# Kernel tuning notes

Measured on AMD Instinct MI355X. Metric: run time of the kernel, lower is better.

Reference implementation:

```python
import jax, jax.numpy as jnp
import numpy as np

N_NODES = 50000
N_EDGES = 800000
D_IN = 128
HID = 128
N_CLS = 5
BN_EPS = 1e-5


def setup_inputs() -> dict:
    key = jax.random.key(0)
    ks = jax.random.split(key, 8)

    def lin(k, fan_in, shape):
        return (jax.random.normal(k, shape, jnp.float32) / np.sqrt(fan_in)).astype(jnp.float32)

    inp = {
        'x': jax.random.normal(ks[0], (N_NODES, D_IN), jnp.float32),
        'edge_index': jax.random.randint(ks[1], (2, N_EDGES), 0, N_NODES, dtype=jnp.int64),
        'W0': lin(ks[2], D_IN, (D_IN, HID)), 'b0': jnp.zeros((HID,), jnp.float32),
        'g0': jnp.ones((HID,), jnp.float32), 'be0': jnp.zeros((HID,), jnp.float32),
        'W1': lin(ks[3], HID, (HID, HID)), 'b1': jnp.zeros((HID,), jnp.float32),
        'g1': jnp.ones((HID,), jnp.float32), 'be1': jnp.zeros((HID,), jnp.float32),
        'W2': lin(ks[4], HID, (HID, HID)), 'b2': jnp.zeros((HID,), jnp.float32),
        'g2': jnp.ones((HID,), jnp.float32), 'be2': jnp.zeros((HID,), jnp.float32),
        'cW1': lin(ks[5], HID, (HID, HID // 2)), 'cb1': jnp.zeros((HID // 2,), jnp.float32),
        'cW2': lin(ks[6], HID // 2, (HID // 2, N_CLS)), 'cb2': jnp.zeros((N_CLS,), jnp.float32),
    }
    return inp


def _gcn_conv(x, src, dst, W, b):
    # H = D~^{-1/2} (A+I) D~^{-1/2} X W + b  (Kipf & Welling / PyG GCNConv)
    h = x @ W                                           # [N, out]
    deg = jnp.zeros((N_NODES,), h.dtype).at[dst].add(1.0) + 1.0  # degree incl. self-loop
    dinv = jax.lax.rsqrt(deg)                           # D~^{-1/2}
    norm = dinv[src] * dinv[dst]                        # [E]
    agg = jnp.zeros_like(h).at[dst].add(h[src] * norm[:, None])
    agg = agg + h * (dinv * dinv)[:, None]              # self-loop term
    return agg + b


def _batchnorm(x, gamma, beta):
    # training-mode BatchNorm1d over the node dimension
    mean = x.mean(axis=0)
    var = x.var(axis=0)
    return gamma * (x - mean) * jax.lax.rsqrt(var + BN_EPS) + beta


def reference(x, edge_index, W0, b0, g0, be0, W1, b1, g1, be1, W2, b2, g2, be2,
              cW1, cb1, cW2, cb2):
    src, dst = edge_index[0], edge_index[1]
    for W, b, g, be in ((W0, b0, g0, be0), (W1, b1, g1, be1), (W2, b2, g2, be2)):
        x = _gcn_conv(x, src, dst, W, b)
        x = _batchnorm(x, g, be)
        x = jax.nn.relu(x)
        # dropout: identity (eval / deterministic reference)
    pooled = x.mean(axis=0, keepdims=True)              # [1, HID]
    h = jax.nn.relu(pooled @ cW1 + cb1)
    return h @ cW2 + cb2                                # [1, N_CLS]
```

## Files before the change

### kernel.cpp

```cpp
#include <hip/hip_runtime.h>
#include <hip/hip_fp16.h>
#include <cstdint>
#include <cstddef>

#define D 128
#define NAGG 2048
#define SCAN_BLOCKS 256


__global__ void count_kernel(const int* __restrict__ ei, int* __restrict__ counts, int E) {
  for (int e = blockIdx.x * blockDim.x + threadIdx.x; e < E; e += gridDim.x * blockDim.x) {
    int d = ei[(size_t)E + e];
    atomicAdd(&counts[d], 1);
  }
}


__global__ __launch_bounds__(256) void scan1_kernel(const int* __restrict__ counts,
                                                    int* __restrict__ blocksums, int N) {
  __shared__ int red[256];
  const int b = blockIdx.x, t = threadIdx.x;
  const int chunk = (N + SCAN_BLOCKS - 1) / SCAN_BLOCKS;
  const int lo = b * chunk, hi = min(lo + chunk, N);
  int s = 0;
  for (int i = lo + t; i < hi; i += 256) s += counts[i];
  red[t] = s;
  __syncthreads();
  for (int off = 128; off > 0; off >>= 1) {
    if (t < off) red[t] += red[t + off];
    __syncthreads();
  }
  if (t == 0) blocksums[b] = red[0];
}

__global__ __launch_bounds__(256) void scan2_kernel(int* __restrict__ blocksums) {
  __shared__ int part[256];
  const int t = threadIdx.x;
  part[t] = blocksums[t];
  __syncthreads();
  for (int off = 1; off < 256; off <<= 1) {
    int v = part[t];
    int u = (t >= off) ? part[t - off] : 0;
    __syncthreads();
    part[t] = v + u;
    __syncthreads();
  }
  blocksums[t] = (t == 0) ? 0 : part[t - 1];
}

__global__ __launch_bounds__(256) void scan3_kernel(const int* __restrict__ counts,
                                                    const int* __restrict__ blocksums,
                                                    int* __restrict__ row_ptr,
                                                    int* __restrict__ cursor,
                                                    float* __restrict__ dinv, int N) {
  __shared__ int tsum[256];
  const int b = blockIdx.x, t = threadIdx.x;
  const int chunk = (N + SCAN_BLOCKS - 1) / SCAN_BLOCKS;
  const int lo = b * chunk, hi = min(lo + chunk, N);
  const int tchunk = (chunk + 255) >> 8;
  const int tlo = lo + t * tchunk, thi = min(tlo + tchunk, hi);
  int s = 0;
  for (int i = tlo; i < thi; i++) s += counts[i];
  tsum[t] = s;
  __syncthreads();
  for (int off = 1; off < 256; off <<= 1) {
    int v = tsum[t];
    int u = (t >= off) ? tsum[t - off] : 0;
    __syncthreads();
    tsum[t] = v + u;
    __syncthreads();
  }
  int run = blocksums[b] + ((t == 0) ? 0 : tsum[t - 1]);
  for (int i = tlo; i < thi; i++) {
    int c = counts[i];
    row_ptr[i] = run; cursor[i] = run; run += c;
    dinv[i] = rsqrtf((float)c + 1.0f);
  }
  if (b == SCAN_BLOCKS - 1 && t == 255) row_ptr[N] = blocksums[b] + tsum[255];
}


__global__ void fill_kernel(const int* __restrict__ ei, int* __restrict__ cursor,
                            int* __restrict__ col, int E) {
  for (int e = blockIdx.x * blockDim.x + threadIdx.x; e < E; e += gridDim.x * blockDim.x) {
    int s = ei[e];
    int d = ei[(size_t)E + e];
    int pos = atomicAdd(&cursor[d], 1);
    atomicExch(&col[pos], s);
  }
}


template <typename T>
__device__ inline float4 load4f(const T* p);
template <>
__device__ inline float4 load4f<float>(const float* p) { return *(const float4*)p; }
template <>
__device__ inline float4 load4f<__half>(const __half* p) {
  float2 a = __half22float2(*(const __half2*)p);
  float2 b = __half22float2(*(const __half2*)(p + 2));
  return make_float4(a.x, a.y, b.x, b.y);
}

template <typename T>
__global__ __launch_bounds__(256) void gemm_kernel(
    const T* __restrict__ A, const float* __restrict__ Wm,
    const float* __restrict__ scale, const float* __restrict__ shift,
    const float* __restrict__ rowscale, __half* __restrict__ out, int M) {
  __shared__ float At[32][132];
  __shared__ float Wl[32][128];
  const int tid = threadIdx.x;
  const int tr = tid >> 4;
  const int tc = tid & 15;
  const int bm = blockIdx.x * 128;

  float acc[8][8];
#pragma unroll
  for (int r = 0; r < 8; r++)
#pragma unroll
    for (int c = 0; c < 8; c++) acc[r][c] = 0.f;

  for (int k0 = 0; k0 < 128; k0 += 32) {
    __syncthreads();
#pragma unroll
    for (int i = 0; i < 4; i++) {
      int idx = tid + i * 256;
      int row = idx >> 3;
      int kk = (idx & 7) << 2;
      int gr = bm + row;
      float4 v = make_float4(0.f, 0.f, 0.f, 0.f);
      if (gr < M) {
        v = load4f(A + (size_t)gr * D + k0 + kk);
        if (scale) {
          int c = k0 + kk;
          v.x = fmaxf(fmaf(v.x, scale[c + 0], shift[c + 0]), 0.f);
          v.y = fmaxf(fmaf(v.y, scale[c + 1], shift[c + 1]), 0.f);
          v.z = fmaxf(fmaf(v.z, scale[c + 2], shift[c + 2]), 0.f);
          v.w = fmaxf(fmaf(v.w, scale[c + 3], shift[c + 3]), 0.f);
        }
      }
      At[kk + 0][row] = v.x; At[kk + 1][row] = v.y;
      At[kk + 2][row] = v.z; At[kk + 3][row] = v.w;
    }
#pragma unroll
    for (int i = 0; i < 4; i++) {
      int idx = tid + i * 256;
      int kk = idx >> 5;
      int c4 = (idx & 31) << 2;
      *(float4*)&Wl[kk][c4] = *(const float4*)(Wm + (size_t)(k0 + kk) * D + c4);
    }
    __syncthreads();

#pragma unroll 4
    for (int kk = 0; kk < 32; kk++) {
      float4 alo = *(const float4*)&At[kk][tr * 8];
      float4 ahi = *(const float4*)&At[kk][tr * 8 + 4];
      float4 blo = *(const float4*)&Wl[kk][tc * 4];
      float4 bhi = *(const float4*)&Wl[kk][tc * 4 + 64];
      float a[8] = {alo.x, alo.y, alo.z, alo.w, ahi.x, ahi.y, ahi.z, ahi.w};
      float b[8] = {blo.x, blo.y, blo.z, blo.w, bhi.x, bhi.y, bhi.z, bhi.w};
#pragma unroll
      for (int r = 0; r < 8; r++)
#pragma unroll
        for (int c = 0; c < 8; c++) acc[r][c] = fmaf(a[r], b[c], acc[r][c]);
    }
  }

#pragma unroll
  for (int r = 0; r < 8; r++) {
    int gr = bm + tr * 8 + r;
    if (gr < M) {
      float dv = rowscale[gr];
      __half2 h0 = __floats2half2_rn(acc[r][0] * dv, acc[r][1] * dv);
      __half2 h1 = __floats2half2_rn(acc[r][2] * dv, acc[r][3] * dv);
      __half2 h2 = __floats2half2_rn(acc[r][4] * dv, acc[r][5] * dv);
      __half2 h3 = __floats2half2_rn(acc[r][6] * dv, acc[r][7] * dv);
      __half2* p0 = (__half2*)(out + (size_t)gr * D + tc * 4);
      __half2* p1 = (__half2*)(out + (size_t)gr * D + tc * 4 + 64);
      p0[0] = h0; p0[1] = h1;
      p1[0] = h2; p1[1] = h3;
    }
  }
}


__global__ __launch_bounds__(256) void agg_kernel(
    const __half* __restrict__ hp, const int* __restrict__ row_ptr, const int* __restrict__ col,
    const float* __restrict__ dinv, const float* __restrict__ bias,
    __half* __restrict__ y, float* __restrict__ pstats, int M) {
  const int tid = threadIdx.x;
  const int wave = tid >> 6;
  const int lane = tid & 63;
  const float bx = bias[lane * 2];
  const float by = bias[lane * 2 + 1];
  float sx = 0.f, sy = 0.f, qx = 0.f, qy = 0.f;

  for (int n = blockIdx.x * 4 + wave; n < M; n += gridDim.x * 4) {
    const int beg = row_ptr[n];
    const int end = row_ptr[n + 1];
    const float dn = dinv[n];
    float2 self = __half22float2(*(const __half2*)(hp + (size_t)n * D + lane * 2));
    float ax = self.x, ay = self.y;
#pragma unroll 4
    for (int e = beg; e < end; e++) {
      int s = col[e];
      float2 hv = __half22float2(*(const __half2*)(hp + (size_t)s * D + lane * 2));
      ax += hv.x; ay += hv.y;
    }
    ax = fmaf(ax, dn, bx);
    ay = fmaf(ay, dn, by);
    *(__half2*)(y + (size_t)n * D + lane * 2) = __floats2half2_rn(ax, ay);
    sx += ax; sy += ay;
    qx = fmaf(ax, ax, qx); qy = fmaf(ay, ay, qy);
  }

  __shared__ float ps[4][128];
  ps[wave][lane * 2] = sx; ps[wave][lane * 2 + 1] = sy;
  __syncthreads();
  if (tid < 128) {
    float s = ps[0][tid] + ps[1][tid] + ps[2][tid] + ps[3][tid];
    pstats[(size_t)blockIdx.x * 256 + tid] = s;
  }
  __syncthreads();
  ps[wave][lane * 2] = qx; ps[wave][lane * 2 + 1] = qy;
  __syncthreads();
  if (tid < 128) {
    float s = ps[0][tid] + ps[1][tid] + ps[2][tid] + ps[3][tid];
    pstats[(size_t)blockIdx.x * 256 + 128 + tid] = s;
  }
}


__global__ void bnred_kernel(const float* __restrict__ pstats, const float* __restrict__ g,
                             const float* __restrict__ be, float* __restrict__ scale,
                             float* __restrict__ shift, float invN) {
  const int c = blockIdx.x;
  const int tid = threadIdx.x;
  float s = 0.f, q = 0.f;
  for (int b = tid; b < NAGG; b += 256) {
    s += pstats[(size_t)b * 256 + c];
    q += pstats[(size_t)b * 256 + 128 + c];
  }
  __shared__ float rs[256], rq[256];
  rs[tid] = s; rq[tid] = q;
  __syncthreads();
  for (int off = 128; off > 0; off >>= 1) {
    if (tid < off) { rs[tid] += rs[tid + off]; rq[tid] += rq[tid + off]; }
    __syncthreads();
  }
  if (tid == 0) {
    float mean = rs[0] * invN;
    float var = rq[0] * invN - mean * mean;
    float sc = g[c] * rsqrtf(var + 1e-5f);
    scale[c] = sc;
    shift[c] = be[c] - mean * sc;
  }
}


__global__ __launch_bounds__(256) void pool_kernel(
    const __half* __restrict__ y, const float* __restrict__ scale, const float* __restrict__ shift,
    float* __restrict__ ppool, int M) {
  const int tid = threadIdx.x;
  const int wave = tid >> 6;
  const int lane = tid & 63;
  const float scx = scale[lane * 2], scy = scale[lane * 2 + 1];
  const float shx = shift[lane * 2], shy = shift[lane * 2 + 1];
  float sx = 0.f, sy = 0.f;
  for (int n = blockIdx.x * 4 + wave; n < M; n += gridDim.x * 4) {
    float2 v = __half22float2(*(const __half2*)(y + (size_t)n * D + lane * 2));
    sx += fmaxf(fmaf(v.x, scx, shx), 0.f);
    sy += fmaxf(fmaf(v.y, scy, shy), 0.f);
  }
  __shared__ float ps[4][128];
  ps[wave][lane * 2] = sx; ps[wave][lane * 2 + 1] = sy;
  __syncthreads();
  if (tid < 128) {
    float s = ps[0][tid] + ps[1][tid] + ps[2][tid] + ps[3][tid];
    ppool[(size_t)blockIdx.x * 128 + tid] = s;
  }
}

__global__ void poolred_kernel(const float* __restrict__ ppool, float* __restrict__ pooled, float invN) {
  const int c = blockIdx.x;
  const int tid = threadIdx.x;
  float s = 0.f;
  for (int b = tid; b < NAGG; b += 256) s += ppool[(size_t)b * 128 + c];
  __shared__ float rs[256];
  rs[tid] = s;
  __syncthreads();
  for (int off = 128; off > 0; off >>= 1) {
    if (tid < off) rs[tid] += rs[tid + off];
    __syncthreads();
  }
  if (tid == 0) pooled[c] = rs[0] * invN;
}


__global__ void mlp_kernel(const float* __restrict__ pooled,
                           const float* __restrict__ cW1, const float* __restrict__ cb1,
                           const float* __restrict__ cW2, const float* __restrict__ cb2,
                           float* __restrict__ outp) {
  __shared__ float pl[128];
  __shared__ float h1[64];
  const int tid = threadIdx.x;
  if (tid < 128) pl[tid] = pooled[tid];
  __syncthreads();
  if (tid < 64) {
    float s = cb1[tid];
    for (int k = 0; k < 128; k++) s = fmaf(pl[k], cW1[(size_t)k * 64 + tid], s);
    h1[tid] = fmaxf(s, 0.f);
  }
  __syncthreads();
  if (tid < 5) {
    float s = cb2[tid];
    for (int k = 0; k < 64; k++) s = fmaf(h1[k], cW2[(size_t)k * 5 + tid], s);
    outp[tid] = s;
  }
}


extern "C" void kernel_launch(void* const* d_in, const int* in_sizes, int n_in,
                              void* d_out, int out_size, void* d_ws, size_t ws_size,
                              hipStream_t stream) {
  const float* x = (const float*)d_in[0];
  const int* ei = (const int*)d_in[1];
  const float* Wm[3] = {(const float*)d_in[2], (const float*)d_in[6], (const float*)d_in[10]};
  const float* bb[3] = {(const float*)d_in[3], (const float*)d_in[7], (const float*)d_in[11]};
  const float* gg[3] = {(const float*)d_in[4], (const float*)d_in[8], (const float*)d_in[12]};
  const float* be[3] = {(const float*)d_in[5], (const float*)d_in[9], (const float*)d_in[13]};
  const float* cW1 = (const float*)d_in[14];
  const float* cb1 = (const float*)d_in[15];
  const float* cW2 = (const float*)d_in[16];
  const float* cb2 = (const float*)d_in[17];
  float* outp = (float*)d_out;

  const int N = in_sizes[0] / D;
  const int E = in_sizes[1] / 2;

  char* wsp = (char*)d_ws;
  size_t off = 0;
  auto alloc = [&](size_t bytes) -> char* {
    char* p = wsp + off;
    off += (bytes + 255) & ~(size_t)255;
    return p;
  };
  int* counts   = (int*)alloc((size_t)N * 4);
  float* dinv   = (float*)alloc((size_t)N * 4);
  int* row_ptr  = (int*)alloc((size_t)(N + 1) * 4);
  int* cursor   = (int*)alloc((size_t)N * 4);
  int* col      = (int*)alloc((size_t)E * 4);
  __half* h     = (__half*)alloc((size_t)N * D * 2);
  __half* y     = (__half*)alloc((size_t)N * D * 2);
  float* pstats = (float*)alloc((size_t)NAGG * 256 * 4);
  float* ppool  = (float*)alloc((size_t)NAGG * 128 * 4);
  float* sc     = (float*)alloc(3 * 128 * 4);
  float* sh     = (float*)alloc(3 * 128 * 4);
  float* pooled = (float*)alloc(128 * 4);
  int* blocksums= (int*)alloc(SCAN_BLOCKS * 4);
  (void)ws_size; (void)n_in; (void)out_size;

  hipMemsetAsync(counts, 0, (size_t)N * 4, stream);
  count_kernel<<<2048, 256, 0, stream>>>(ei, counts, E);
  scan1_kernel<<<SCAN_BLOCKS, 256, 0, stream>>>(counts, blocksums, N);
  scan2_kernel<<<1, 256, 0, stream>>>(blocksums);
  scan3_kernel<<<SCAN_BLOCKS, 256, 0, stream>>>(counts, blocksums, row_ptr, cursor, dinv, N);
  fill_kernel<<<2048, 256, 0, stream>>>(ei, cursor, col, E);

  const int gblocks = (N + 127) / 128;
  const float invN = 1.0f / (float)N;
  for (int L = 0; L < 3; L++) {
    const float* scl = (L == 0) ? nullptr : sc + (size_t)(L - 1) * 128;
    const float* shf = (L == 0) ? nullptr : sh + (size_t)(L - 1) * 128;
    if (L == 0)
      gemm_kernel<float><<<gblocks, 256, 0, stream>>>(x, Wm[L], scl, shf, dinv, h, N);
    else
      gemm_kernel<__half><<<gblocks, 256, 0, stream>>>(y, Wm[L], scl, shf, dinv, h, N);
    agg_kernel<<<NAGG, 256, 0, stream>>>(h, row_ptr, col, dinv, bb[L], y, pstats, N);
    bnred_kernel<<<128, 256, 0, stream>>>(pstats, gg[L], be[L], sc + (size_t)L * 128,
                                          sh + (size_t)L * 128, invN);
  }
  pool_kernel<<<NAGG, 256, 0, stream>>>(y, sc + 256, sh + 256, ppool, N);
  poolred_kernel<<<128, 256, 0, stream>>>(ppool, pooled, invN);
  mlp_kernel<<<1, 128, 0, stream>>>(pooled, cW1, cb1, cW2, cb2, outp);
}
```

Before: 455.8 us.

## Replace FP32 SIMT GEMM with FP16 MFMA GEMM using swizzled LDS tiles

Swaps the scalar FP32 register-tiled GEMM for a matrix-core kernel built on mfma_f32_16x16x16f16. A and the full 128-wide K panel are staged in LDS as FP16 with an XOR swizzle to avoid bank conflicts. A new prep kernel converts and transposes the three weight matrices to FP16 once per call. The fill kernel also replaces atomicExch with a plain store. Converting the layer-0 input and the weights to FP16 lowers precision, and the epilogue now writes scalar halves instead of packed vectors.

```diff
diff --git a/kernel.cpp b/kernel.cpp
--- a/kernel.cpp
+++ b/kernel.cpp
@@ -7,6 +7,13 @@
 #define NAGG 2048
 #define SCAN_BLOCKS 256
 
+using f16x4 = __attribute__((ext_vector_type(4))) _Float16;
+using f32x4 = __attribute__((ext_vector_type(4))) float;
+
+__device__ __forceinline__ int swz(int row, int byte) {
+  return row * 256 + (((byte)&0xF0) ^ ((row & 7) << 4)) + ((byte)&0x0F);
+}
+
 
 __global__ void count_kernel(const int* __restrict__ ei, int* __restrict__ counts, int E) {
   for (int e = blockIdx.x * blockDim.x + threadIdx.x; e < E; e += gridDim.x * blockDim.x) {
@@ -14,7 +21,6 @@
     atomicAdd(&counts[d], 1);
   }
 }
-
 
 __global__ __launch_bounds__(256) void scan1_kernel(const int* __restrict__ counts,
                                                     int* __restrict__ blocksums, int N) {
@@ -86,99 +92,118 @@
     int s = ei[e];
     int d = ei[(size_t)E + e];
     int pos = atomicAdd(&cursor[d], 1);
-    atomicExch(&col[pos], s);
-  }
+    col[pos] = s;
+  }
+}
+
+
+__global__ void wconv_kernel(const float* __restrict__ W0, const float* __restrict__ W1,
+                             const float* __restrict__ W2, __half* __restrict__ Wt) {
+  int i = blockIdx.x * 256 + threadIdx.x;
+  if (i >= 3 * 128 * 128) return;
+  int L = i >> 14, r = i & 16383;
+  int col = r >> 7, k = r & 127;
+  const float* W = (L == 0) ? W0 : (L == 1) ? W1 : W2;
+  Wt[i] = __float2half(W[k * 128 + col]);
 }
 
 
 template <typename T>
-__device__ inline float4 load4f(const T* p);
-template <>
-__device__ inline float4 load4f<float>(const float* p) { return *(const float4*)p; }
-template <>
-__device__ inline float4 load4f<__half>(const __half* p) {
-  float2 a = __half22float2(*(const __half2*)p);
-  float2 b = __half22float2(*(const __half2*)(p + 2));
-  return make_float4(a.x, a.y, b.x, b.y);
-}
-
-template <typename T>
-__global__ __launch_bounds__(256) void gemm_kernel(
-    const T* __restrict__ A, const float* __restrict__ Wm,
+__global__ __launch_bounds__(256, 2) void gemm_mfma_kernel(
+    const T* __restrict__ A, const __half* __restrict__ Wt,
     const float* __restrict__ scale, const float* __restrict__ shift,
-    const float* __restrict__ rowscale, __half* __restrict__ out, int M) {
-  __shared__ float At[32][132];
-  __shared__ float Wl[32][128];
-  const int tid = threadIdx.x;
-  const int tr = tid >> 4;
-  const int tc = tid & 15;
+    const float* __restrict__ dinv, __half* __restrict__ out, int M) {
+  __shared__ __align__(16) char asb[128 * 256];
+  __shared__ __align__(16) char bsb[128 * 256];
+  const int tid = threadIdx.x;
   const int bm = blockIdx.x * 128;
 
-  float acc[8][8];
-#pragma unroll
-  for (int r = 0; r < 8; r++)
-#pragma unroll
-    for (int c = 0; c < 8; c++) acc[r][c] = 0.f;
-
-  for (int k0 = 0; k0 < 128; k0 += 32) {
-    __syncthreads();
-#pragma unroll
-    for (int i = 0; i < 4; i++) {
-      int idx = tid + i * 256;
-      int row = idx >> 3;
-      int kk = (idx & 7) << 2;
+  if constexpr (sizeof(T) == 4) {
+    for (int i = 0; i < 16; i++) {
+      int g = tid + i * 256;
+      int row = g >> 5;
+      int c4 = (g & 31) << 2;
       int gr = bm + row;
       float4 v = make_float4(0.f, 0.f, 0.f, 0.f);
+      if (gr < M) v = *(const float4*)(A + (size_t)gr * D + c4);
+      union { float2 f2; __half h[4]; } u;
+      u.h[0] = __float2half(v.x); u.h[1] = __float2half(v.y);
+      u.h[2] = __float2half(v.z); u.h[3] = __float2half(v.w);
+      *(float2*)(asb + swz(row, c4 * 2)) = u.f2;
+    }
+  } else {
+    for (int i = 0; i < 8; i++) {
+      int g = tid + i * 256;
+      int row = g >> 4;
+      int c8 = (g & 15) << 3;
+      int gr = bm + row;
+      union { float4 f4; __half h[8]; } u;
       if (gr < M) {
-        v = load4f(A + (size_t)gr * D + k0 + kk);
-        if (scale) {
-          int c = k0 + kk;
-          v.x = fmaxf(fmaf(v.x, scale[c + 0], shift[c + 0]), 0.f);
-          v.y = fmaxf(fmaf(v.y, scale[c + 1], shift[c + 1]), 0.f);
-          v.z = fmaxf(fmaf(v.z, scale[c + 2], shift[c + 2]), 0.f);
-          v.w = fmaxf(fmaf(v.w, scale[c + 3], shift[c + 3]), 0.f);
-        }
+        u.f4 = *(const float4*)((const __half*)A + (size_t)gr * D + c8);
+        float4 s0 = *(const float4*)&scale[c8];
+        float4 s1 = *(const float4*)&scale[c8 + 4];
+        float4 b0 = *(const float4*)&shift[c8];
+        float4 b1 = *(const float4*)&shift[c8 + 4];
+        const float* sp = &s0.x; const float* bp = &b0.x;
+#pragma unroll
+        for (int j = 0; j < 4; j++)
+          u.h[j] = __float2half(fmaxf(fmaf(__half2float(u.h[j]), sp[j], bp[j]), 0.f));
+        sp = &s1.x; bp = &b1.x;
+#pragma unroll
+        for (int j = 0; j < 4; j++)
+          u.h[4 + j] = __float2half(fmaxf(fmaf(__half2float(u.h[4 + j]), sp[j], bp[j]), 0.f));
+      } else {
+        u.f4 = make_float4(0.f, 0.f, 0.f, 0.f);
       }
-      At[kk + 0][row] = v.x; At[kk + 1][row] = v.y;
-      At[kk + 2][row] = v.z; At[kk + 3][row] = v.w;
+      *(float4*)(asb + swz(row, c8 * 2)) = u.f4;
     }
-#pragma unroll
-    for (int i = 0; i < 4; i++) {
-      int idx = tid + i * 256;
-      int kk = idx >> 5;
-      int c4 = (idx & 31) << 2;
-      *(float4*)&Wl[kk][c4] = *(const float4*)(Wm + (size_t)(k0 + kk) * D + c4);
+  }
+  for (int i = 0; i < 8; i++) {
+    int g = tid + i * 256;
+    int row = g >> 3;
+    int sl = (g & 7) << 4;
+    *(float4*)(bsb + swz(row, sl)) = *(const float4*)((const char*)Wt + (size_t)g * 16);
+  }
+  __syncthreads();
+
+  const int lane = tid & 63;
+  const int w = tid >> 6;
+  const int l15 = lane & 15;
+  const int khalf = lane >> 4;
+
+  f32x4 acc[2][8];
+#pragma unroll
+  for (int m = 0; m < 2; m++)
+#pragma unroll
+    for (int n = 0; n < 8; n++) acc[m][n] = (f32x4){0.f, 0.f, 0.f, 0.f};
+
+#pragma unroll
+  for (int ks = 0; ks < 8; ks++) {
+    int kbyte = ks * 32 + khalf * 8;
+    f16x4 a0 = *(const f16x4*)(asb + swz(w * 32 + l15, kbyte));
+    f16x4 a1 = *(const f16x4*)(asb + swz(w * 32 + 16 + l15, kbyte));
+#pragma unroll
+    for (int n = 0; n < 8; n++) {
+      f16x4 b = *(const f16x4*)(bsb + swz(n * 16 + l15, kbyte));
+      acc[0][n] = __builtin_amdgcn_mfma_f32_16x16x16f16(a0, b, acc[0][n], 0, 0, 0);
+      acc[1][n] = __builtin_amdgcn_mfma_f32_16x16x16f16(a1, b, acc[1][n], 0, 0, 0);
     }
-    __syncthreads();
-
-#pragma unroll 4
-    for (int kk = 0; kk < 32; kk++) {
-      float4 alo = *(const float4*)&At[kk][tr * 8];
-      float4 ahi = *(const float4*)&At[kk][tr * 8 + 4];
-      float4 blo = *(const float4*)&Wl[kk][tc * 4];
-      float4 bhi = *(const float4*)&Wl[kk][tc * 4 + 64];
-      float a[8] = {alo.x, alo.y, alo.z, alo.w, ahi.x, ahi.y, ahi.z, ahi.w};
-      float b[8] = {blo.x, blo.y, blo.z, blo.w, bhi.x, bhi.y, bhi.z, bhi.w};
-#pragma unroll
-      for (int r = 0; r < 8; r++)
-#pragma unroll
-        for (int c = 0; c < 8; c++) acc[r][c] = fmaf(a[r], b[c], acc[r][c]);
-    }
-  }
-
-#pragma unroll
-  for (int r = 0; r < 8; r++) {
-    int gr = bm + tr * 8 + r;
-    if (gr < M) {
-      float dv = rowscale[gr];
-      __half2 h0 = __floats2half2_rn(acc[r][0] * dv, acc[r][1] * dv);
-      __half2 h1 = __floats2half2_rn(acc[r][2] * dv, acc[r][3] * dv);
-      __half2 h2 = __floats2half2_rn(acc[r][4] * dv, acc[r][5] * dv);
-      __half2 h3 = __floats2half2_rn(acc[r][6] * dv, acc[r][7] * dv);
-      __half2* p0 = (__half2*)(out + (size_t)gr * D + tc * 4);
-      __half2* p1 = (__half2*)(out + (size_t)gr * D + tc * 4 + 64);
-      p0[0] = h0; p0[1] = h1;
-      p1[0] = h2; p1[1] = h3;
+  }
+
+#pragma unroll
+  for (int m = 0; m < 2; m++) {
+    int base_r = bm + w * 32 + m * 16 + khalf * 4;
+    float dv[4];
+#pragma unroll
+    for (int j = 0; j < 4; j++) dv[j] = (base_r + j < M) ? dinv[base_r + j] : 0.f;
+#pragma unroll
+    for (int n = 0; n < 8; n++) {
+      int colg = n * 16 + l15;
+#pragma unroll
+      for (int j = 0; j < 4; j++) {
+        int r = base_r + j;
+        if (r < M) out[(size_t)r * D + colg] = __float2half(acc[m][n][j] * dv[j]);
+      }
     }
   }
 }
@@ -352,6 +377,7 @@
   int* col      = (int*)alloc((size_t)E * 4);
   __half* h     = (__half*)alloc((size_t)N * D * 2);
   __half* y     = (__half*)alloc((size_t)N * D * 2);
+  __half* Wt    = (__half*)alloc((size_t)3 * 128 * 128 * 2);
   float* pstats = (float*)alloc((size_t)NAGG * 256 * 4);
   float* ppool  = (float*)alloc((size_t)NAGG * 128 * 4);
   float* sc     = (float*)alloc(3 * 128 * 4);
@@ -361,6 +387,7 @@
   (void)ws_size; (void)n_in; (void)out_size;
 
   hipMemsetAsync(counts, 0, (size_t)N * 4, stream);
+  wconv_kernel<<<192, 256, 0, stream>>>(Wm[0], Wm[1], Wm[2], Wt);
   count_kernel<<<2048, 256, 0, stream>>>(ei, counts, E);
   scan1_kernel<<<SCAN_BLOCKS, 256, 0, stream>>>(counts, blocksums, N);
   scan2_kernel<<<1, 256, 0, stream>>>(blocksums);
@@ -373,9 +400,9 @@
     const float* scl = (L == 0) ? nullptr : sc + (size_t)(L - 1) * 128;
     const float* shf = (L == 0) ? nullptr : sh + (size_t)(L - 1) * 128;
     if (L == 0)
-      gemm_kernel<float><<<gblocks, 256, 0, stream>>>(x, Wm[L], scl, shf, dinv, h, N);
+      gemm_mfma_kernel<float><<<gblocks, 256, 0, stream>>>(x, Wt, scl, shf, dinv, h, N);
     else
-      gemm_kernel<__half><<<gblocks, 256, 0, stream>>>(y, Wm[L], scl, shf, dinv, h, N);
+      gemm_mfma_kernel<__half><<<gblocks, 256, 0, stream>>>(y, Wt + (size_t)L * 16384, scl, shf, dinv, h, N);
     agg_kernel<<<NAGG, 256, 0, stream>>>(h, row_ptr, col, dinv, bb[L], y, pstats, N);
     bnred_kernel<<<128, 256, 0, stream>>>(pstats, gg[L], be[L], sc + (size_t)L * 128,
                                           sh + (size_t)L * 128, invN);
```

After: 421.0 us. -7.6%, faster.
